# Performance work log

Measured on AMD Instinct MI355X. Metric: run time of the kernel, lower is better.

The kernel has to match this reference:

```python
import jax, jax.numpy as jnp
import numpy as np

EPS = 1e-5

def setup_inputs() -> dict:
    key = jax.random.key(0)
    ks = jax.random.split(key, 10)
    B, C, H, W = 4, 512, 56, 56
    n_heads = 8
    nq = H * W
    oq = (H // 2) * (W // 2)  # sr_ratio=2, k=3,s=2,p=1 -> halved spatial dims
    s = 0.02
    return {
        'x': jax.random.normal(ks[0], (B, C, H, W), jnp.float32),
        'attn_weights': jax.random.uniform(ks[1], (B, n_heads, nq, oq), jnp.float32),
        'q_w': jax.random.normal(ks[2], (C, C), jnp.float32) * s,
        'k_w': jax.random.normal(ks[3], (C, C), jnp.float32) * s,
        'v_w': jax.random.normal(ks[4], (C, C), jnp.float32) * s,
        'sr_w': jax.random.normal(ks[5], (C, 1, 3, 3), jnp.float32) * s,  # depthwise OIHW
        'sr_b': jnp.zeros((C,), jnp.float32),
        'ln_g': jnp.ones((C,), jnp.float32),
        'ln_b': jnp.zeros((C,), jnp.float32),
        'tc_w': jax.random.normal(ks[6], (n_heads, n_heads), jnp.float32) * 0.3,  # 1x1 conv over heads
        'tc_b': jnp.zeros((n_heads,), jnp.float32),
        'proj_w': jax.random.normal(ks[7], (C, C), jnp.float32) * s,
        'proj_b': jnp.zeros((C,), jnp.float32),
    }

def _layernorm(x, g, b):
    m = jnp.mean(x, axis=-1, keepdims=True)
    v = jnp.var(x, axis=-1, keepdims=True)
    return (x - m) * jax.lax.rsqrt(v + EPS) * g + b

def reference(x, attn_weights, q_w, k_w, v_w, sr_w, sr_b, ln_g, ln_b, tc_w, tc_b, proj_w, proj_b):
    B, C, H, W = x.shape
    n_heads = tc_w.shape[0]
    hd = C // n_heads
    scale = hd ** -0.5
    nq = H * W
    xf = x.reshape(B, C, nq).transpose(0, 2, 1)  # (B, nq, C)
    q = (xf @ q_w.T).reshape(B, nq, n_heads, hd).transpose(0, 2, 1, 3)  # (B, h, nq, hd)
    # spatial reduction: depthwise conv k=3, s=2, p=1 on NCHW, then LayerNorm
    xs = jax.lax.conv_general_dilated(
        x, sr_w, window_strides=(2, 2), padding=((1, 1), (1, 1)),
        feature_group_count=C, dimension_numbers=('NCHW', 'OIHW', 'NCHW'))
    xs = xs + sr_b[None, :, None, None]
    oq = xs.shape[2] * xs.shape[3]
    xs = xs.reshape(B, C, oq).transpose(0, 2, 1)  # (B, oq, C)
    xs = _layernorm(xs, ln_g, ln_b)
    k = (xs @ k_w.T).reshape(B, oq, n_heads, hd).transpose(0, 2, 3, 1)  # (B, h, hd, oq)
    v = (xs @ v_w.T).reshape(B, oq, n_heads, hd).transpose(0, 2, 1, 3)  # (B, h, oq, hd)
    attn = jnp.einsum('bhqd,bhdo->bhqo', q, k) * scale  # (B, h, nq, oq)
    # apply_transform: 1x1 conv mixing heads -> softmax -> InstanceNorm2d (no affine)
    attn = jnp.einsum('bhqo,gh->bgqo', attn, tc_w) + tc_b[None, :, None, None]
    attn = jax.nn.softmax(attn, axis=-1)
    m = jnp.mean(attn, axis=(2, 3), keepdims=True)
    var = jnp.var(attn, axis=(2, 3), keepdims=True)
    attn = (attn - m) * jax.lax.rsqrt(var + EPS)
    attn = attn_weights * attn
    out = jnp.einsum('bhqo,bhod->bhqd', attn, v)  # (B, h, nq, hd)
    out = out.transpose(0, 2, 1, 3).reshape(B, nq, C)
    out = out @ proj_w.T + proj_b
    return out.reshape(B, H, W, C).transpose(0, 3, 1, 2)
```

## Files before the change

### kernel.cpp

```cpp
#include <hip/hip_runtime.h>

typedef _Float16 half8 __attribute__((ext_vector_type(8)));
typedef _Float16 half4 __attribute__((ext_vector_type(4)));
typedef float fx4 __attribute__((ext_vector_type(4)));

#define MFMA16(a,b,c) __builtin_amdgcn_mfma_f32_16x16x32_f16(a,b,c,0,0,0)

#define BN 4
#define CC 512
#define HH 56
#define WW 56
#define NQ 3136
#define OQ 784
#define NH 8
#define HD 64
#define NSEG 7
#define BGN (BN * NH * NQ)

__device__ inline half8 h8z() {
    half8 v;
#pragma unroll
    for (int j = 0; j < 8; j++) v[j] = (_Float16)0.f;
    return v;
}

__global__ void cvt4_kernel(const float* __restrict__ a, const float* __restrict__ b,
                            const float* __restrict__ c, const float* __restrict__ d,
                            _Float16* __restrict__ o, float* __restrict__ S2) {
    if (blockIdx.x == 0 && blockIdx.y == 0 && threadIdx.x < 32) S2[threadIdx.x] = 0.f;
    int y = blockIdx.y;
    const float* s = (y == 0) ? a : (y == 1) ? b : (y == 2) ? c : d;
    int i = blockIdx.x * 256 + threadIdx.x;
    o[(size_t)y * 262144 + i] = (_Float16)s[i];
}

__global__ void xpose_kernel(const float* __restrict__ x, _Float16* __restrict__ xf) {
    __shared__ float t[32][33];
    int n0 = blockIdx.x * 32, c0 = blockIdx.y * 32, b = blockIdx.z;
    int tx = threadIdx.x, ty = threadIdx.y;
#pragma unroll
    for (int i = 0; i < 4; i++)
        t[ty + 8 * i][tx] = x[((size_t)(b * CC) + c0 + ty + 8 * i) * NQ + n0 + tx];
    __syncthreads();
#pragma unroll
    for (int i = 0; i < 4; i++)
        xf[((size_t)(b * NQ) + n0 + ty + 8 * i) * CC + c0 + tx] = (_Float16)t[tx][ty + 8 * i];
}

__global__ void dw_kernel(const float* __restrict__ x, const float* __restrict__ w,
                          const float* __restrict__ bias, float* __restrict__ xsc) {
    int cb = blockIdx.x, oy = blockIdx.y, b = blockIdx.z;
    int tx = threadIdx.x, ty = threadIdx.y;
    int c = cb * 16 + ty;
    float a = bias[c];
    const float* xp = x + ((size_t)(b * CC + c) * HH) * WW;
#pragma unroll
    for (int ky = 0; ky < 3; ky++) {
        int iy = 2 * oy - 1 + ky;
        if (iy < 0 || iy >= HH) continue;
#pragma unroll
        for (int kx = 0; kx < 3; kx++) {
            int ix = 2 * tx - 1 + kx;
            if (ix < 0 || ix >= WW) continue;
            a += xp[iy * WW + ix] * w[c * 9 + ky * 3 + kx];
        }
    }
    __shared__ float tile[28][17];
    tile[tx][ty] = a;
    __syncthreads();
    int lin = ty * 28 + tx;
    int oi = lin >> 4, ci = lin & 15;
    xsc[((size_t)(b * OQ) + oy * 28 + oi) * CC + cb * 16 + ci] = tile[oi][ci];
}

__global__ __launch_bounds__(256) void ln_kernel(const float* __restrict__ xsc,
        const float* __restrict__ g, const float* __restrict__ bb,
        _Float16* __restrict__ xs16) {
    int row = blockIdx.x;
    const float* rp = xsc + (size_t)row * CC;
    int t = threadIdx.x;
    float v0 = rp[t], v1 = rp[t + 256];
    float s = v0 + v1, ss = v0 * v0 + v1 * v1;
#pragma unroll
    for (int m = 1; m < 64; m <<= 1) {
        s += __shfl_xor(s, m, 64);
        ss += __shfl_xor(ss, m, 64);
    }
    __shared__ float red[8];
    int wv = t >> 6;
    if ((t & 63) == 0) { red[wv] = s; red[4 + wv] = ss; }
    __syncthreads();
    s = red[0] + red[1] + red[2] + red[3];
    ss = red[4] + red[5] + red[6] + red[7];
    float mean = s * (1.f / 512.f);
    float var = ss * (1.f / 512.f) - mean * mean;
    float rs = rsqrtf(var + 1e-5f);
    xs16[(size_t)row * CC + t] = (_Float16)((v0 - mean) * rs * g[t] + bb[t]);
    xs16[(size_t)row * CC + t + 256] = (_Float16)((v1 - mean) * rs * g[t + 256] + bb[t + 256]);
}

__global__ __launch_bounds__(256) void gemm_qkv(const _Float16* __restrict__ xf,
        const _Float16* __restrict__ xs, const _Float16* __restrict__ w4,
        _Float16* __restrict__ q16, _Float16* __restrict__ k16, _Float16* __restrict__ vT) {
    const int which = blockIdx.z;
    if (which && blockIdx.x >= 49) return;
    const _Float16* A = which ? xs : xf;
    const _Float16* Bw = w4 + (size_t)which * 262144;
    __shared__ _Float16 As[64 * 72];
    __shared__ _Float16 Bs[64 * 72];
    const int m0 = blockIdx.x * 64, n0 = blockIdx.y * 64;
    const int tid = threadIdx.x;
    const int lane = tid & 63, wv = tid >> 6;
    const int wm = (wv >> 1) * 32, wn = (wv & 1) * 32;
    const int l15 = lane & 15, quad = lane >> 4;
    fx4 acc[2][2];
#pragma unroll
    for (int i = 0; i < 2; i++)
#pragma unroll
        for (int j = 0; j < 2; j++) acc[i][j] = fx4{0.f, 0.f, 0.f, 0.f};
    for (int k0 = 0; k0 < 512; k0 += 64) {
        __syncthreads();
#pragma unroll
        for (int i = 0; i < 2; i++) {
            int id = tid + 256 * i;
            int r = id >> 3, kc = (id & 7) << 3;
            *(half8*)(As + r * 72 + kc) = *(const half8*)(A + (size_t)(m0 + r) * 512 + k0 + kc);
            *(half8*)(Bs + r * 72 + kc) = *(const half8*)(Bw + (size_t)(n0 + r) * 512 + k0 + kc);
        }
        __syncthreads();
#pragma unroll
        for (int ks = 0; ks < 2; ks++) {
            half8 af[2], bf[2];
#pragma unroll
            for (int s = 0; s < 2; s++) {
                af[s] = *(const half8*)(As + (wm + s * 16 + l15) * 72 + ks * 32 + quad * 8);
                bf[s] = *(const half8*)(Bs + (wn + s * 16 + l15) * 72 + ks * 32 + quad * 8);
            }
#pragma unroll
            for (int i = 0; i < 2; i++)
#pragma unroll
                for (int j = 0; j < 2; j++)
                    acc[i][j] = MFMA16(af[i], bf[j], acc[i][j]);
        }
    }
    if (which < 2) {
        _Float16* O = which ? k16 : q16;
#pragma unroll
        for (int i = 0; i < 2; i++)
#pragma unroll
            for (int j = 0; j < 2; j++) {
                int col = n0 + wn + j * 16 + l15;
#pragma unroll
                for (int e = 0; e < 4; e++) {
                    int row = m0 + wm + i * 16 + quad * 4 + e;
                    O[(size_t)row * 512 + col] = (_Float16)acc[i][j][e];
                }
            }
    } else {
#pragma unroll
        for (int i = 0; i < 2; i++) {
            int row = m0 + wm + i * 16 + quad * 4;
            int b = row / OQ;
            int o = row - b * OQ;
#pragma unroll
            for (int j = 0; j < 2; j++) {
                int c = n0 + wn + j * 16 + l15;
                half4 pk;
#pragma unroll
                for (int e = 0; e < 4; e++) pk[e] = (_Float16)acc[i][j][e];
                *(half4*)(vT + ((size_t)(b * NH + (c >> 6)) * HD + (c & 63)) * OQ + o) = pk;
            }
        }
    }
}

__global__ __launch_bounds__(256) void qk_mix(const _Float16* __restrict__ q16,
        const _Float16* __restrict__ k16, const float* __restrict__ tcw,
        const float* __restrict__ tcb, _Float16* __restrict__ L,
        float* __restrict__ Zpart, float* __restrict__ E2part) {
    __shared__ _Float16 kl[16 * 520];
    __shared__ float tcs[64];
    __shared__ float tbb[8];
    const int b = blockIdx.z, oseg = blockIdx.y, ob = oseg * 112;
    const int tid = threadIdx.x;
    const int wv = tid >> 6, lane = tid & 63, l15 = lane & 15, quad = lane >> 4;
    const int n0 = blockIdx.x * 64 + wv * 16;
    if (tid < 64) tcs[tid] = tcw[tid] * 0.125f;
    else if (tid < 72) tbb[tid - 64] = tcb[tid - 64];

    half8 aF[8][2];
    const _Float16* qrow = q16 + ((size_t)(b * NQ + n0 + l15)) * 512;
#pragma unroll
    for (int h = 0; h < 8; h++)
#pragma unroll
        for (int ks = 0; ks < 2; ks++)
            aF[h][ks] = *(const half8*)(qrow + h * 64 + ks * 32 + quad * 8);

    float z[8][4], s2[8][4];
#pragma unroll
    for (int g = 0; g < 8; g++)
#pragma unroll
        for (int e = 0; e < 4; e++) { z[g][e] = 0.f; s2[g][e] = 0.f; }

    for (int ot = 0; ot < 7; ot++) {
        int o0 = ob + ot * 16;
        __syncthreads();
        const _Float16* kb = k16 + ((size_t)(b * OQ + o0)) * 512;
#pragma unroll
        for (int i = 0; i < 4; i++) {
            int id = tid + 256 * i;
            int r = id >> 6, c = (id & 63) << 3;
            *(half8*)(kl + r * 520 + c) = *(const half8*)(kb + (size_t)r * 512 + c);
        }
        __syncthreads();
        fx4 s[8];
#pragma unroll
        for (int h = 0; h < 8; h++) {
            fx4 a = fx4{0.f, 0.f, 0.f, 0.f};
#pragma unroll
            for (int ks = 0; ks < 2; ks++) {
                half8 bF = *(const half8*)(kl + l15 * 520 + h * 64 + ks * 32 + quad * 8);
                a = MFMA16(aF[h][ks], bF, a);
            }
            s[h] = a;
        }
#pragma unroll
        for (int g = 0; g < 8; g++) {
#pragma unroll
            for (int e = 0; e < 4; e++) {
                float v = tbb[g];
#pragma unroll
                for (int h = 0; h < 8; h++) v += tcs[g * 8 + h] * s[h][e];
                _Float16 vh = (_Float16)v;
                float vr = (float)vh;
                float ex = __expf(vr);
                z[g][e] += ex;
                s2[g][e] += ex * ex;
                L[((size_t)((b * 8 + g) * NQ) + n0 + quad * 4 + e) * OQ + o0 + l15] = vh;
            }
        }
    }
#pragma unroll
    for (int m = 1; m < 16; m <<= 1) {
#pragma unroll
        for (int g = 0; g < 8; g++)
#pragma unroll
            for (int e = 0; e < 4; e++) {
                z[g][e] += __shfl_xor(z[g][e], m, 64);
                s2[g][e] += __shfl_xor(s2[g][e], m, 64);
            }
    }
    if (l15 < 8) {
        int g = l15;
        size_t base = (size_t)oseg * BGN + (size_t)(b * 8 + g) * NQ + n0 + quad * 4;
#pragma unroll
        for (int e = 0; e < 4; e++) {
            Zpart[base + e] = z[g][e];
            E2part[base + e] = s2[g][e];
        }
    }
}

__global__ __launch_bounds__(256) void zfin_kernel(const float* __restrict__ Zpart,
        const float* __restrict__ E2part, float* __restrict__ Zinv, float* __restrict__ S2) {
    int i = blockIdx.x * 256 + threadIdx.x;
    float z = 0.f, e2 = 0.f;
#pragma unroll
    for (int s = 0; s < NSEG; s++) {
        z += Zpart[(size_t)s * BGN + i];
        e2 += E2part[(size_t)s * BGN + i];
    }
    float zi = 1.f / z;
    Zinv[i] = zi;
    float r = e2 * zi * zi;
#pragma unroll
    for (int m = 1; m < 64; m <<= 1) r += __shfl_xor(r, m, 64);
    if ((threadIdx.x & 63) == 0) atomicAdd(&S2[i / NQ], r);
}

__global__ __launch_bounds__(64) void pv_kernel(const _Float16* __restrict__ L,
        const float* __restrict__ W, const _Float16* __restrict__ vT,
        const float* __restrict__ Zinv, const float* __restrict__ S2,
        _Float16* __restrict__ outp) {
    const int b = blockIdx.z, n0 = blockIdx.x * 16, g = blockIdx.y;
    const int lane = threadIdx.x, l15 = lane & 15, quad = lane >> 4;
    const int bg = b * 8 + g;
    const float mm = 1.f / (float)OQ;
    float rv = rsqrtf(S2[bg] * (1.f / ((float)NQ * (float)OQ)) - mm * mm + 1e-5f);
    const float czr = Zinv[bg * NQ + n0 + l15] * rv;
    const float rm = rv * mm;
    const _Float16* Lrow = L + ((size_t)bg * NQ + n0 + l15) * OQ;
    const float* Wrow = W + ((size_t)bg * NQ + n0 + l15) * OQ;
    const _Float16* vb = vT + (size_t)bg * HD * OQ;
    fx4 acc[4];
#pragma unroll
    for (int d = 0; d < 4; d++) acc[d] = fx4{0.f, 0.f, 0.f, 0.f};

#pragma unroll 5
    for (int oc = 0; oc < 25; oc++) {
        int kbase = oc * 32 + quad * 8;
        bool valid = kbase < OQ;
        half8 aH = h8z();
        if (valid) {
            half8 l8 = *(const half8*)(Lrow + kbase);
            fx4 w0 = *(const fx4*)(Wrow + kbase);
            fx4 w1 = *(const fx4*)(Wrow + kbase + 4);
#pragma unroll
            for (int j = 0; j < 8; j++) {
                float e = __expf((float)l8[j]);
                float a = e * czr - rm;
                float wv = (j < 4) ? w0[j] : w1[j - 4];
                aH[j] = (_Float16)(a * wv);
            }
        }
#pragma unroll
        for (int ds = 0; ds < 4; ds++) {
            half8 bF = h8z();
            if (valid)
                bF = *(const half8*)(vb + ((size_t)(ds * 16 + l15)) * OQ + kbase);
            acc[ds] = MFMA16(aH, bF, acc[ds]);
        }
    }
#pragma unroll
    for (int ds = 0; ds < 4; ds++)
#pragma unroll
        for (int e = 0; e < 4; e++) {
            int n = n0 + quad * 4 + e;
            int c = g * 64 + ds * 16 + l15;
            outp[((size_t)b * NQ + n) * 512 + c] = (_Float16)acc[ds][e];
        }
}

__global__ __launch_bounds__(256) void gemm_proj(const _Float16* __restrict__ A,
        const _Float16* __restrict__ Ball, const float* __restrict__ bias,
        float* __restrict__ Oall) {
    __shared__ _Float16 As[64 * 72];
    __shared__ _Float16 Bs[64 * 72];
    const int b = blockIdx.z;
    const _Float16* Bm = Ball + (size_t)b * NQ * 512;
    float* O = Oall + (size_t)b * CC * NQ;
    const int m0 = blockIdx.x * 64, n0 = blockIdx.y * 64;
    const int tid = threadIdx.x;
    const int lane = tid & 63, wv = tid >> 6;
    const int wm = (wv >> 1) * 32, wn = (wv & 1) * 32;
    const int l15 = lane & 15, quad = lane >> 4;
    fx4 acc[2][2];
#pragma unroll
    for (int i = 0; i < 2; i++)
#pragma unroll
        for (int j = 0; j < 2; j++) acc[i][j] = fx4{0.f, 0.f, 0.f, 0.f};
    for (int k0 = 0; k0 < 512; k0 += 64) {
        __syncthreads();
#pragma unroll
        for (int i = 0; i < 2; i++) {
            int id = tid + 256 * i;
            int r = id >> 3, kc = (id & 7) << 3;
            *(half8*)(As + r * 72 + kc) = *(const half8*)(A + (size_t)(m0 + r) * 512 + k0 + kc);
            *(half8*)(Bs + r * 72 + kc) = *(const half8*)(Bm + (size_t)(n0 + r) * 512 + k0 + kc);
        }
        __syncthreads();
#pragma unroll
        for (int ks = 0; ks < 2; ks++) {
            half8 af[2], bf[2];
#pragma unroll
            for (int s = 0; s < 2; s++) {
                af[s] = *(const half8*)(As + (wm + s * 16 + l15) * 72 + ks * 32 + quad * 8);
                bf[s] = *(const half8*)(Bs + (wn + s * 16 + l15) * 72 + ks * 32 + quad * 8);
            }
#pragma unroll
            for (int i = 0; i < 2; i++)
#pragma unroll
                for (int j = 0; j < 2; j++)
                    acc[i][j] = MFMA16(af[i], bf[j], acc[i][j]);
        }
    }
#pragma unroll
    for (int i = 0; i < 2; i++)
#pragma unroll
        for (int j = 0; j < 2; j++) {
            int col = n0 + wn + j * 16 + l15;
#pragma unroll
            for (int e = 0; e < 4; e++) {
                int row = m0 + wm + i * 16 + quad * 4 + e;
                O[(size_t)row * NQ + col] = acc[i][j][e] + bias[row];
            }
        }
}

extern "C" void kernel_launch(void* const* d_in, const int* in_sizes, int n_in,
                              void* d_out, int out_size, void* d_ws, size_t ws_size,
                              hipStream_t stream) {
    const float* x = (const float*)d_in[0];
    const float* aw = (const float*)d_in[1];
    const float* q_w = (const float*)d_in[2];
    const float* k_w = (const float*)d_in[3];
    const float* v_w = (const float*)d_in[4];
    const float* sr_w = (const float*)d_in[5];
    const float* sr_b = (const float*)d_in[6];
    const float* ln_g = (const float*)d_in[7];
    const float* ln_b = (const float*)d_in[8];
    const float* tc_w = (const float*)d_in[9];
    const float* tc_b = (const float*)d_in[10];
    const float* p_w = (const float*)d_in[11];
    const float* p_b = (const float*)d_in[12];
    float* out = (float*)d_out;

    char* p = (char*)d_ws;
    auto take = [&](size_t bytes) -> char* {
        char* r = p;
        p += (bytes + 255) & ~(size_t)255;
        return r;
    };
    _Float16* qw16 = (_Float16*)take(512 * 512 * 2);
    _Float16* kw16 = (_Float16*)take(512 * 512 * 2);
    _Float16* vw16 = (_Float16*)take(512 * 512 * 2);
    _Float16* pw16 = (_Float16*)take(512 * 512 * 2);
    _Float16* xf16 = (_Float16*)take((size_t)BN * NQ * CC * 2);
    float* xsc = (float*)take((size_t)BN * OQ * CC * 4);
    _Float16* xs16 = (_Float16*)take((size_t)BN * OQ * CC * 2);
    _Float16* q16 = (_Float16*)take((size_t)BN * NQ * CC * 2);
    _Float16* k16 = (_Float16*)take((size_t)BN * OQ * CC * 2);
    _Float16* vT = (_Float16*)take((size_t)BN * OQ * CC * 2);
    _Float16* outp = (_Float16*)take((size_t)BN * NQ * CC * 2);
    float* Zpart = (float*)take((size_t)NSEG * BGN * 4);
    float* E2part = (float*)take((size_t)NSEG * BGN * 4);
    float* S2 = (float*)take(32 * 4);
    float* Zinv = (float*)take((size_t)BGN * 4);
    _Float16* L = (_Float16*)take((size_t)BN * NH * NQ * OQ * 2);

    cvt4_kernel<<<dim3(1024, 4), 256, 0, stream>>>(q_w, k_w, v_w, p_w, qw16, S2);
    xpose_kernel<<<dim3(98, 16, BN), dim3(32, 8), 0, stream>>>(x, xf16);
    dw_kernel<<<dim3(32, 28, BN), dim3(28, 16), 0, stream>>>(x, sr_w, sr_b, xsc);
    ln_kernel<<<BN * OQ, 256, 0, stream>>>(xsc, ln_g, ln_b, xs16);
    gemm_qkv<<<dim3(196, 8, 3), 256, 0, stream>>>(xf16, xs16, qw16, q16, k16, vT);
    qk_mix<<<dim3(49, 7, BN), 256, 0, stream>>>(q16, k16, tc_w, tc_b, L, Zpart, E2part);
    zfin_kernel<<<BGN / 256, 256, 0, stream>>>(Zpart, E2part, Zinv, S2);
    pv_kernel<<<dim3(196, 8, BN), 64, 0, stream>>>(L, aw, vT, Zinv, S2, outp);
    gemm_proj<<<dim3(8, 49, BN), 256, 0, stream>>>(pw16, outp, p_b, out);
}
```

Before: 792.7 us.

## Tile attention logits and weights into 32-wide chunks for coalesced PV loads

A new wrelay_kernel converts attn_weights from fp32 to fp16 and writes them in a tiled [bg][chunk][nq][32] layout, padding the tail with zeros. qk_mix now writes the logits L in the same tiled layout. pv_kernel can then read contiguous 32-element chunks of both L and W without per-iteration bounds checks. The aim is to cut PV-stage load traffic and improve coalescing. In exchange it adds a full extra pass over attn_weights, an fp16 rounding of the weights, and unmasked tail reads of L and vT, where uninitialised padding could produce NaN.

```diff
diff --git a/kernel.cpp b/kernel.cpp
--- a/kernel.cpp
+++ b/kernel.cpp
@@ -15,6 +15,7 @@
 #define NH 8
 #define HD 64
 #define NSEG 7
+#define NOC 25
 #define BGN (BN * NH * NQ)
 
 __device__ inline half8 h8z() {
@@ -97,6 +98,30 @@
     float rs = rsqrtf(var + 1e-5f);
     xs16[(size_t)row * CC + t] = (_Float16)((v0 - mean) * rs * g[t] + bb[t]);
     xs16[(size_t)row * CC + t + 256] = (_Float16)((v1 - mean) * rs * g[t + 256] + bb[t + 256]);
+}
+
+__global__ __launch_bounds__(256) void wrelay_kernel(const float* __restrict__ W,
+                                                     _Float16* __restrict__ Wt) {
+    __shared__ _Float16 wl[32][800];
+    const int bg = blockIdx.y, n0 = blockIdx.x * 32;
+    const int tid = threadIdx.x;
+    for (int i = tid; i < 32 * 196; i += 256) {
+        int r = i / 196, c = i - r * 196;
+        fx4 v = *(const fx4*)(W + ((size_t)bg * NQ + n0 + r) * OQ + c * 4);
+        half4 h;
+#pragma unroll
+        for (int j = 0; j < 4; j++) h[j] = (_Float16)v[j];
+        *(half4*)(&wl[r][c * 4]) = h;
+    }
+    for (int i = tid; i < 32 * 16; i += 256)
+        wl[i >> 4][784 + (i & 15)] = (_Float16)0.f;
+    __syncthreads();
+    for (int j = tid; j < NOC * 256; j += 256) {
+        int oc = j >> 8, t = j & 255;
+        int r = t >> 3, o = (t & 7) * 4;
+        half4 h = *(half4*)(&wl[r][oc * 32 + o]);
+        *(half4*)(Wt + (((size_t)bg * NOC + oc) * NQ + n0 + r) * 32 + o) = h;
+    }
 }
 
 __global__ __launch_bounds__(256) void gemm_qkv(const _Float16* __restrict__ xf,
@@ -176,7 +201,7 @@
 
 __global__ __launch_bounds__(256) void qk_mix(const _Float16* __restrict__ q16,
         const _Float16* __restrict__ k16, const float* __restrict__ tcw,
-        const float* __restrict__ tcb, _Float16* __restrict__ L,
+        const float* __restrict__ tcb, _Float16* __restrict__ Lt,
         float* __restrict__ Zpart, float* __restrict__ E2part) {
     __shared__ _Float16 kl[16 * 520];
     __shared__ float tcs[64];
@@ -224,8 +249,10 @@
             }
             s[h] = a;
         }
+        const int oc = o0 >> 5, oi = (o0 & 31) + l15;
 #pragma unroll
         for (int g = 0; g < 8; g++) {
+            size_t tbase = (((size_t)(b * 8 + g) * NOC + oc) * NQ + n0 + quad * 4) * 32 + oi;
 #pragma unroll
             for (int e = 0; e < 4; e++) {
                 float v = tbb[g];
@@ -236,7 +263,7 @@
                 float ex = __expf(vr);
                 z[g][e] += ex;
                 s2[g][e] += ex * ex;
-                L[((size_t)((b * 8 + g) * NQ) + n0 + quad * 4 + e) * OQ + o0 + l15] = vh;
+                Lt[tbase + (size_t)e * 32] = vh;
             }
         }
     }
@@ -278,8 +305,8 @@
     if ((threadIdx.x & 63) == 0) atomicAdd(&S2[i / NQ], r);
 }
 
-__global__ __launch_bounds__(64) void pv_kernel(const _Float16* __restrict__ L,
-        const float* __restrict__ W, const _Float16* __restrict__ vT,
+__global__ __launch_bounds__(64) void pv_kernel(const _Float16* __restrict__ Lt,
+        const _Float16* __restrict__ Wt, const _Float16* __restrict__ vT,
         const float* __restrict__ Zinv, const float* __restrict__ S2,
         _Float16* __restrict__ outp) {
     const int b = blockIdx.z, n0 = blockIdx.x * 16, g = blockIdx.y;
@@ -289,35 +316,29 @@
     float rv = rsqrtf(S2[bg] * (1.f / ((float)NQ * (float)OQ)) - mm * mm + 1e-5f);
     const float czr = Zinv[bg * NQ + n0 + l15] * rv;
     const float rm = rv * mm;
-    const _Float16* Lrow = L + ((size_t)bg * NQ + n0 + l15) * OQ;
-    const float* Wrow = W + ((size_t)bg * NQ + n0 + l15) * OQ;
+    const size_t tstride = (size_t)NQ * 32;
+    const size_t rowoff = (size_t)(n0 + l15) * 32 + quad * 8;
+    const _Float16* Lp = Lt + (size_t)bg * NOC * tstride + rowoff;
+    const _Float16* Wp = Wt + (size_t)bg * NOC * tstride + rowoff;
     const _Float16* vb = vT + (size_t)bg * HD * OQ;
     fx4 acc[4];
 #pragma unroll
     for (int d = 0; d < 4; d++) acc[d] = fx4{0.f, 0.f, 0.f, 0.f};
 
 #pragma unroll 5
-    for (int oc = 0; oc < 25; oc++) {
-        int kbase = oc * 32 + quad * 8;
-        bool valid = kbase < OQ;
-        half8 aH = h8z();
-        if (valid) {
-            half8 l8 = *(const half8*)(Lrow + kbase);
-            fx4 w0 = *(const fx4*)(Wrow + kbase);
-            fx4 w1 = *(const fx4*)(Wrow + kbase + 4);
-#pragma unroll
-            for (int j = 0; j < 8; j++) {
-                float e = __expf((float)l8[j]);
-                float a = e * czr - rm;
-                float wv = (j < 4) ? w0[j] : w1[j - 4];
-                aH[j] = (_Float16)(a * wv);
-            }
-        }
+    for (int oc = 0; oc < NOC; oc++) {
+        half8 l8 = *(const half8*)(Lp + oc * tstride);
+        half8 w8 = *(const half8*)(Wp + oc * tstride);
+        half8 aH;
+#pragma unroll
+        for (int j = 0; j < 8; j++) {
+            float e = __expf((float)l8[j]);
+            aH[j] = (_Float16)((e * czr - rm) * (float)w8[j]);
+        }
+        int kb = oc * 32 + quad * 8;
 #pragma unroll
         for (int ds = 0; ds < 4; ds++) {
-            half8 bF = h8z();
-            if (valid)
-                bF = *(const half8*)(vb + ((size_t)(ds * 16 + l15)) * OQ + kbase);
+            half8 bF = *(const half8*)(vb + (size_t)(ds * 16 + l15) * OQ + kb);
             acc[ds] = MFMA16(aH, bF, acc[ds]);
         }
     }
@@ -426,15 +447,17 @@
     float* E2part = (float*)take((size_t)NSEG * BGN * 4);
     float* S2 = (float*)take(32 * 4);
     float* Zinv = (float*)take((size_t)BGN * 4);
-    _Float16* L = (_Float16*)take((size_t)BN * NH * NQ * OQ * 2);
+    _Float16* Lt = (_Float16*)take((size_t)32 * NOC * NQ * 32 * 2);
+    _Float16* Wt = (_Float16*)take((size_t)32 * NOC * NQ * 32 * 2);
 
     cvt4_kernel<<<dim3(1024, 4), 256, 0, stream>>>(q_w, k_w, v_w, p_w, qw16, S2);
+    wrelay_kernel<<<dim3(98, 32), 256, 0, stream>>>(aw, Wt);
     xpose_kernel<<<dim3(98, 16, BN), dim3(32, 8), 0, stream>>>(x, xf16);
     dw_kernel<<<dim3(32, 28, BN), dim3(28, 16), 0, stream>>>(x, sr_w, sr_b, xsc);
     ln_kernel<<<BN * OQ, 256, 0, stream>>>(xsc, ln_g, ln_b, xs16);
     gemm_qkv<<<dim3(196, 8, 3), 256, 0, stream>>>(xf16, xs16, qw16, q16, k16, vT);
-    qk_mix<<<dim3(49, 7, BN), 256, 0, stream>>>(q16, k16, tc_w, tc_b, L, Zpart, E2part);
+    qk_mix<<<dim3(49, 7, BN), 256, 0, stream>>>(q16, k16, tc_w, tc_b, Lt, Zpart, E2part);
     zfin_kernel<<<BGN / 256, 256, 0, stream>>>(Zpart, E2part, Zinv, S2);
-    pv_kernel<<<dim3(196, 8, BN), 64, 0, stream>>>(L, aw, vT, Zinv, S2, outp);
+    pv_kernel<<<dim3(196, 8, BN), 64, 0, stream>>>(Lt, Wt, vT, Zinv, S2, outp);
     gemm_proj<<<dim3(8, 49, BN), 256, 0, stream>>>(pw16, outp, p_b, out);
 }
```

Measured after the change: 810.9 us. 2.3% more time.

## Recompute QK logits in PV kernel instead of materializing L; relay W as fp16 tiles

Applied to the files above, without the earlier changes.

The stats kernel no longer writes the large fp16 logit tensor L. The PV kernel now recomputes QK and the head mix per tile, applies exp, normalisation and the attention weights, and accumulates all 8 heads per block, split over two o-segments whose partial outputs are summed in gemm_proj. Extra blocks in the stats kernel convert the fp32 attn_weights into fp16 tiles in a permuted, MFMA-friendly layout. This removes a roughly 200MB write and read round trip, at the cost of recomputing the QK MFMAs, a much smaller PV grid with heavy register use, and fp16 rounding of the weights and of exp.

```diff
diff --git a/kernel.cpp b/kernel.cpp
--- a/kernel.cpp
+++ b/kernel.cpp
@@ -15,6 +15,8 @@
 #define NH 8
 #define HD 64
 #define NSEG 7
+#define NOC 25
+#define NTILE 196
 #define BGN (BN * NH * NQ)
 
 __device__ inline half8 h8z() {
@@ -174,15 +176,48 @@
     }
 }
 
-__global__ __launch_bounds__(256) void qk_mix(const _Float16* __restrict__ q16,
-        const _Float16* __restrict__ k16, const float* __restrict__ tcw,
-        const float* __restrict__ tcb, _Float16* __restrict__ L,
+__global__ __launch_bounds__(256) void qkstats_wrelay(
+        const _Float16* __restrict__ q16, const _Float16* __restrict__ k16,
+        const float* __restrict__ tcw, const float* __restrict__ tcb,
+        const float* __restrict__ W, _Float16* __restrict__ Wt,
         float* __restrict__ Zpart, float* __restrict__ E2part) {
-    __shared__ _Float16 kl[16 * 520];
+    __shared__ _Float16 shbuf[12800];
     __shared__ float tcs[64];
     __shared__ float tbb[8];
+    const int tid = threadIdx.x;
+    if (blockIdx.y >= NSEG) {
+        _Float16 (*wl)[800] = (_Float16(*)[800])shbuf;
+        int blk = (blockIdx.z * 8 + (blockIdx.y - NSEG)) * 49 + blockIdx.x;
+#pragma unroll 1
+        for (int i = 0; i < 4; i++) {
+            int u = blk * 4 + i;
+            int nb = u % NTILE;
+            int bg = u / NTILE;
+            int b = bg >> 3, g = bg & 7;
+            if (i) __syncthreads();
+            for (int j = tid; j < 16 * 196; j += 256) {
+                int r = j / 196, c = j - r * 196;
+                fx4 v = *(const fx4*)(W + ((size_t)bg * NQ + nb * 16 + r) * OQ + c * 4);
+                half4 h;
+#pragma unroll
+                for (int t = 0; t < 4; t++) h[t] = (_Float16)v[t];
+                *(half4*)(&wl[r][c * 4]) = h;
+            }
+            for (int j = tid; j < 16 * 16; j += 256)
+                wl[j >> 4][784 + (j & 15)] = (_Float16)0.f;
+            __syncthreads();
+            for (int j = tid; j < NOC * 64; j += 256) {
+                int oc = j >> 6, t = j & 63;
+                int n = t >> 2, o8 = (t & 3) * 8;
+                half8 h = *(half8*)(&wl[n][oc * 32 + o8]);
+                *(half8*)(Wt + ((size_t)(((b * NTILE + nb) * NOC + oc) * 8 + g)) * 512
+                          + n * 32 + o8) = h;
+            }
+        }
+        return;
+    }
+    _Float16* kl = shbuf;
     const int b = blockIdx.z, oseg = blockIdx.y, ob = oseg * 112;
-    const int tid = threadIdx.x;
     const int wv = tid >> 6, lane = tid & 63, l15 = lane & 15, quad = lane >> 4;
     const int n0 = blockIdx.x * 64 + wv * 16;
     if (tid < 64) tcs[tid] = tcw[tid] * 0.125f;
@@ -232,11 +267,9 @@
 #pragma unroll
                 for (int h = 0; h < 8; h++) v += tcs[g * 8 + h] * s[h][e];
                 _Float16 vh = (_Float16)v;
-                float vr = (float)vh;
-                float ex = __expf(vr);
+                float ex = __expf((float)vh);
                 z[g][e] += ex;
                 s2[g][e] += ex * ex;
-                L[((size_t)((b * 8 + g) * NQ) + n0 + quad * 4 + e) * OQ + o0 + l15] = vh;
             }
         }
     }
@@ -278,66 +311,131 @@
     if ((threadIdx.x & 63) == 0) atomicAdd(&S2[i / NQ], r);
 }
 
-__global__ __launch_bounds__(64) void pv_kernel(const _Float16* __restrict__ L,
-        const float* __restrict__ W, const _Float16* __restrict__ vT,
+__global__ __launch_bounds__(256, 2) void pv2_kernel(
+        const _Float16* __restrict__ q16, const _Float16* __restrict__ k16,
+        const _Float16* __restrict__ Wt, const _Float16* __restrict__ vT,
+        const float* __restrict__ tcw, const float* __restrict__ tcb,
         const float* __restrict__ Zinv, const float* __restrict__ S2,
-        _Float16* __restrict__ outp) {
-    const int b = blockIdx.z, n0 = blockIdx.x * 16, g = blockIdx.y;
-    const int lane = threadIdx.x, l15 = lane & 15, quad = lane >> 4;
-    const int bg = b * 8 + g;
+        _Float16* __restrict__ outP) {
+    __shared__ _Float16 kl[16 * 520];
+    __shared__ _Float16 pt[4 * 8 * 16 * 40];
+    __shared__ float tcs[64];
+    __shared__ float tbb[8];
+    const int b = blockIdx.z, nb = blockIdx.x, oseg = blockIdx.y;
+    const int tid = threadIdx.x;
+    const int wv = tid >> 6, lane = tid & 63, l15 = lane & 15, quad = lane >> 4;
+    const int n0 = nb * 64 + wv * 16;
+    const int nbt = nb * 4 + wv;
+    if (tid < 64) tcs[tid] = tcw[tid] * 0.125f;
+    else if (tid < 72) tbb[tid - 64] = tcb[tid - 64];
     const float mm = 1.f / (float)OQ;
-    float rv = rsqrtf(S2[bg] * (1.f / ((float)NQ * (float)OQ)) - mm * mm + 1e-5f);
-    const float czr = Zinv[bg * NQ + n0 + l15] * rv;
-    const float rm = rv * mm;
-    const _Float16* Lrow = L + ((size_t)bg * NQ + n0 + l15) * OQ;
-    const float* Wrow = W + ((size_t)bg * NQ + n0 + l15) * OQ;
-    const _Float16* vb = vT + (size_t)bg * HD * OQ;
-    fx4 acc[4];
-#pragma unroll
-    for (int d = 0; d < 4; d++) acc[d] = fx4{0.f, 0.f, 0.f, 0.f};
-
-#pragma unroll 5
-    for (int oc = 0; oc < 25; oc++) {
-        int kbase = oc * 32 + quad * 8;
-        bool valid = kbase < OQ;
-        half8 aH = h8z();
-        if (valid) {
-            half8 l8 = *(const half8*)(Lrow + kbase);
-            fx4 w0 = *(const fx4*)(Wrow + kbase);
-            fx4 w1 = *(const fx4*)(Wrow + kbase + 4);
-#pragma unroll
-            for (int j = 0; j < 8; j++) {
-                float e = __expf((float)l8[j]);
-                float a = e * czr - rm;
-                float wv = (j < 4) ? w0[j] : w1[j - 4];
-                aH[j] = (_Float16)(a * wv);
-            }
-        }
-#pragma unroll
-        for (int ds = 0; ds < 4; ds++) {
-            half8 bF = h8z();
-            if (valid)
-                bF = *(const half8*)(vb + ((size_t)(ds * 16 + l15)) * OQ + kbase);
-            acc[ds] = MFMA16(aH, bF, acc[ds]);
-        }
-    }
-#pragma unroll
-    for (int ds = 0; ds < 4; ds++)
-#pragma unroll
-        for (int e = 0; e < 4; e++) {
-            int n = n0 + quad * 4 + e;
-            int c = g * 64 + ds * 16 + l15;
-            outp[((size_t)b * NQ + n) * 512 + c] = (_Float16)acc[ds][e];
-        }
+    float czr[8], rm[8];
+#pragma unroll
+    for (int g = 0; g < 8; g++) {
+        int bg = b * 8 + g;
+        float rv = rsqrtf(S2[bg] * (1.f / ((float)NQ * (float)OQ)) - mm * mm + 1e-5f);
+        czr[g] = Zinv[(size_t)bg * NQ + n0 + l15] * rv;
+        rm[g] = rv * mm;
+    }
+    fx4 acc[8][4];
+#pragma unroll
+    for (int g = 0; g < 8; g++)
+#pragma unroll
+        for (int d = 0; d < 4; d++) acc[g][d] = fx4{0.f, 0.f, 0.f, 0.f};
+    const int ocS = oseg ? 13 : 0, ocE = oseg ? 25 : 13;
+    const _Float16* qrow = q16 + (size_t)(b * NQ + n0 + l15) * 512;
+    _Float16* ptw = pt + wv * (8 * 16 * 40);
+
+#pragma unroll 1
+    for (int oc = ocS; oc < ocE; oc++) {
+#pragma unroll
+        for (int hf = 0; hf < 2; hf++) {
+            const int o0 = oc * 32 + hf * 16;
+            const bool val = o0 < OQ;
+            __syncthreads();
+            if (val) {
+                const _Float16* kb = k16 + (size_t)(b * OQ + o0) * 512;
+#pragma unroll
+                for (int i = 0; i < 4; i++) {
+                    int id = tid + 256 * i;
+                    int r = id >> 6, c = (id & 63) << 3;
+                    *(half8*)(kl + r * 520 + c) = *(const half8*)(kb + (size_t)r * 512 + c);
+                }
+            }
+            __syncthreads();
+            if (val) {
+                fx4 s[8];
+#pragma unroll
+                for (int h = 0; h < 8; h++) {
+                    half8 a0 = *(const half8*)(qrow + h * 64 + quad * 8);
+                    half8 a1 = *(const half8*)(qrow + h * 64 + 32 + quad * 8);
+                    half8 b0 = *(const half8*)(kl + l15 * 520 + h * 64 + quad * 8);
+                    half8 b1 = *(const half8*)(kl + l15 * 520 + h * 64 + 32 + quad * 8);
+                    fx4 a = fx4{0.f, 0.f, 0.f, 0.f};
+                    a = MFMA16(a0, b0, a);
+                    a = MFMA16(a1, b1, a);
+                    s[h] = a;
+                }
+#pragma unroll
+                for (int g = 0; g < 8; g++) {
+#pragma unroll
+                    for (int e = 0; e < 4; e++) {
+                        float v = tbb[g];
+#pragma unroll
+                        for (int h = 0; h < 8; h++) v += tcs[g * 8 + h] * s[h][e];
+                        _Float16 vh = (_Float16)v;
+                        float ex = __expf((float)vh);
+                        ptw[(g * 16 + quad * 4 + e) * 40 + hf * 16 + l15] = (_Float16)ex;
+                    }
+                }
+            } else {
+#pragma unroll
+                for (int g = 0; g < 8; g++)
+#pragma unroll
+                    for (int e = 0; e < 4; e++)
+                        ptw[(g * 16 + quad * 4 + e) * 40 + hf * 16 + l15] = (_Float16)0.f;
+            }
+        }
+        const int kb32 = oc * 32 + quad * 8;
+#pragma unroll
+        for (int g = 0; g < 8; g++) {
+            half8 aP = *(const half8*)(ptw + (g * 16 + l15) * 40 + quad * 8);
+            half8 w8 = *(const half8*)(Wt
+                + ((size_t)(((b * NTILE + nbt) * NOC + oc) * 8 + g)) * 512
+                + l15 * 32 + quad * 8);
+            half8 aH;
+#pragma unroll
+            for (int j = 0; j < 8; j++)
+                aH[j] = (_Float16)(((float)aP[j] * czr[g] - rm[g]) * (float)w8[j]);
+            const _Float16* vb = vT + (size_t)(b * 8 + g) * HD * OQ;
+#pragma unroll
+            for (int ds = 0; ds < 4; ds++) {
+                half8 bF = *(const half8*)(vb + (size_t)(ds * 16 + l15) * OQ + kb32);
+                acc[g][ds] = MFMA16(aH, bF, acc[g][ds]);
+            }
+        }
+    }
+    _Float16* op = outP + (size_t)oseg * BN * NQ * 512;
+#pragma unroll
+    for (int g = 0; g < 8; g++)
+#pragma unroll
+        for (int ds = 0; ds < 4; ds++)
+#pragma unroll
+            for (int e = 0; e < 4; e++) {
+                int n = n0 + quad * 4 + e;
+                int c = g * 64 + ds * 16 + l15;
+                op[((size_t)b * NQ + n) * 512 + c] = (_Float16)acc[g][ds][e];
+            }
 }
 
 __global__ __launch_bounds__(256) void gemm_proj(const _Float16* __restrict__ A,
-        const _Float16* __restrict__ Ball, const float* __restrict__ bias,
+        const _Float16* __restrict__ outP, const float* __restrict__ bias,
         float* __restrict__ Oall) {
     __shared__ _Float16 As[64 * 72];
     __shared__ _Float16 Bs[64 * 72];
     const int b = blockIdx.z;
-    const _Float16* Bm = Ball + (size_t)b * NQ * 512;
+    const _Float16* P0 = outP + (size_t)b * NQ * 512;
+    const _Float16* P1 = outP + (size_t)BN * NQ * 512 + (size_t)b * NQ * 512;
     float* O = Oall + (size_t)b * CC * NQ;
     const int m0 = blockIdx.x * 64, n0 = blockIdx.y * 64;
     const int tid = threadIdx.x;
@@ -356,7 +454,12 @@
             int id = tid + 256 * i;
             int r = id >> 3, kc = (id & 7) << 3;
             *(half8*)(As + r * 72 + kc) = *(const half8*)(A + (size_t)(m0 + r) * 512 + k0 + kc);
-            *(half8*)(Bs + r * 72 + kc) = *(const half8*)(Bm + (size_t)(n0 + r) * 512 + k0 + kc);
+            half8 b0 = *(const half8*)(P0 + (size_t)(n0 + r) * 512 + k0 + kc);
+            half8 b1 = *(const half8*)(P1 + (size_t)(n0 + r) * 512 + k0 + kc);
+            half8 vb;
+#pragma unroll
+            for (int j = 0; j < 8; j++) vb[j] = (_Float16)((float)b0[j] + (float)b1[j]);
+            *(half8*)(Bs + r * 72 + kc) = vb;
         }
         __syncthreads();
 #pragma unroll
@@ -421,20 +524,22 @@
     _Float16* q16 = (_Float16*)take((size_t)BN * NQ * CC * 2);
     _Float16* k16 = (_Float16*)take((size_t)BN * OQ * CC * 2);
     _Float16* vT = (_Float16*)take((size_t)BN * OQ * CC * 2);
-    _Float16* outp = (_Float16*)take((size_t)BN * NQ * CC * 2);
+    _Float16* outP = (_Float16*)take((size_t)2 * BN * NQ * CC * 2);
     float* Zpart = (float*)take((size_t)NSEG * BGN * 4);
     float* E2part = (float*)take((size_t)NSEG * BGN * 4);
     float* S2 = (float*)take(32 * 4);
     float* Zinv = (float*)take((size_t)BGN * 4);
-    _Float16* L = (_Float16*)take((size_t)BN * NH * NQ * OQ * 2);
+    _Float16* Wt = (_Float16*)take((size_t)BN * NTILE * NOC * 8 * 512 * 2);
 
     cvt4_kernel<<<dim3(1024, 4), 256, 0, stream>>>(q_w, k_w, v_w, p_w, qw16, S2);
     xpose_kernel<<<dim3(98, 16, BN), dim3(32, 8), 0, stream>>>(x, xf16);
     dw_kernel<<<dim3(32, 28, BN), dim3(28, 16), 0, stream>>>(x, sr_w, sr_b, xsc);
     ln_kernel<<<BN * OQ, 256, 0, stream>>>(xsc, ln_g, ln_b, xs16);
     gemm_qkv<<<dim3(196, 8, 3), 256, 0, stream>>>(xf16, xs16, qw16, q16, k16, vT);
-    qk_mix<<<dim3(49, 7, BN), 256, 0, stream>>>(q16, k16, tc_w, tc_b, L, Zpart, E2part);
+    qkstats_wrelay<<<dim3(49, NSEG + 8, BN), 256, 0, stream>>>(
+        q16, k16, tc_w, tc_b, aw, Wt, Zpart, E2part);
     zfin_kernel<<<BGN / 256, 256, 0, stream>>>(Zpart, E2part, Zinv, S2);
-    pv_kernel<<<dim3(196, 8, BN), 64, 0, stream>>>(L, aw, vT, Zinv, S2, outp);
-    gemm_proj<<<dim3(8, 49, BN), 256, 0, stream>>>(pw16, outp, p_b, out);
-}
+    pv2_kernel<<<dim3(49, 2, BN), 256, 0, stream>>>(
+        q16, k16, Wt, vT, tc_w, tc_b, Zinv, S2, outP);
+    gemm_proj<<<dim3(8, 49, BN), 256, 0, stream>>>(pw16, outP, p_b, out);
+}
```

Measured after the change: 894.6 us. +12.8%, slower.
